# Performance work log

Measured on AMD Instinct MI355X. Metric: run time of the kernel, lower is better.

## Reference

```python
import jax, jax.numpy as jnp
import numpy as np

N = 8192      # number of tokens (input_dim in the original code)
D = 512       # hidden/embedding dim
R = 20        # number of dependency labels (2R with reverses)
L = 2         # num_layers
OUT = 256     # output_dim


def setup_inputs() -> dict:
    key = jax.random.key(0)
    ks = jax.random.split(key, 10)
    s = 0.02
    return {
        "x": jax.random.normal(ks[0], (N, D), dtype=jnp.float32),
        "dep_idx": jax.random.randint(ks[1], (N,), 0, N, dtype=jnp.int32),
        "rel_idx": jax.random.randint(ks[2], (N,), 0, R, dtype=jnp.int32),
        "gov_idx": jax.random.randint(ks[3], (N,), 0, N, dtype=jnp.int32),
        "W_self": jax.random.normal(ks[4], (L, D, D), dtype=jnp.float32) * s,
        "b_self": jax.random.normal(ks[5], (L, D), dtype=jnp.float32) * s,
        "W_rel": jax.random.normal(ks[6], (L, 2 * R, D, D), dtype=jnp.float32) * s,
        "b_rel": jax.random.normal(ks[7], (L, 2 * R, D), dtype=jnp.float32) * s,
        "W_ff": jax.random.normal(ks[8], (OUT, D), dtype=jnp.float32) * s,
        "b_ff": jax.random.normal(ks[9], (OUT,), dtype=jnp.float32) * s,
    }


def _gcn_layer(x, dep_idx, rel_idx, gov_idx, Ws, bs, Wr, br):
    # self transform applied to every token: temp[idx] = W_self @ x[idx] + b
    out = x @ Ws.T + bs  # [N, D]
    # relation-specific message passing: loop over the small fixed label set.
    # For each relation r: transform ALL nodes once (dense GEMM), then
    # mask-gather-scatter only the edges carrying that relation.
    for r in range(R):
        m = (rel_idx == r)[:, None]                      # [E, 1]
        # forward direction: dependent += W_r @ x[governor] + b_r
        h_f = x @ Wr[r].T + br[r]                        # [N, D]
        out = out.at[dep_idx].add(jnp.where(m, h_f[gov_idx], 0.0))
        # reverse direction: governor += W_{r}_r @ x[dependent] + b
        h_b = x @ Wr[R + r].T + br[R + r]                # [N, D]
        out = out.at[gov_idx].add(jnp.where(m, h_b[dep_idx], 0.0))
    return jax.nn.relu(out)


def reference(x, dep_idx, rel_idx, gov_idx, W_self, b_self, W_rel, b_rel, W_ff, b_ff):
    h = x
    for l in range(L):  # dropout_rate=0.0 -> dropout is identity; last layer has no dropout anyway
        h = _gcn_layer(h, dep_idx, rel_idx, gov_idx, W_self[l], b_self[l], W_rel[l], b_rel[l])
    return h @ W_ff.T + b_ff  # [N, OUT]
```

## Files before the change

kernel.cpp:

```cpp
#include <hip/hip_runtime.h>

#define N_TOK 8192
#define DIM   512
#define NREL  20
#define NGRP  40
#define OUTD  256
#define STILE 64
#define MAXT  168
#define MAXP  (MAXT*128)

typedef unsigned short u16;
typedef u16    u16x8  __attribute__((ext_vector_type(8)));
typedef __bf16 bf16x8 __attribute__((ext_vector_type(8)));
typedef float  f32x4  __attribute__((ext_vector_type(4)));

__device__ __forceinline__ u16 f2bf(float f) {
  union { float f; unsigned u; } v; v.f = f;
  return (u16)((v.u + 0x7FFFu + ((v.u >> 16) & 1u)) >> 16);
}

__global__ void k_cvt4(const float* __restrict__ s0, u16* __restrict__ d0, int m0,
                       const float* __restrict__ s1, u16* __restrict__ d1, int m1,
                       const float* __restrict__ s2, u16* __restrict__ d2, int m2,
                       const float* __restrict__ s3, u16* __restrict__ d3, int m3) {
  const int stride = gridDim.x * blockDim.x;
  const int t0 = blockIdx.x * blockDim.x + threadIdx.x;
#define CVT_LOOP(S, D, N)                                                    \
  for (int i = t0; i < N; i += stride) {                                     \
    float4 v = reinterpret_cast<const float4*>(S)[i];                        \
    reinterpret_cast<ushort4*>(D)[i] =                                       \
        make_ushort4(f2bf(v.x), f2bf(v.y), f2bf(v.z), f2bf(v.w));            \
  }
  CVT_LOOP(s0, d0, m0) CVT_LOOP(s1, d1, m1) CVT_LOOP(s2, d2, m2) CVT_LOOP(s3, d3, m3)
#undef CVT_LOOP
}

__global__ void k_cvtr(const float* __restrict__ in, u16* __restrict__ out, int n4) {
  const int stride = gridDim.x * blockDim.x;
  for (int i = blockIdx.x * blockDim.x + threadIdx.x; i < n4; i += stride) {
    float4 v = reinterpret_cast<const float4*>(in)[i];
    reinterpret_cast<ushort4*>(out)[i] =
        make_ushort4(f2bf(fmaxf(v.x, 0.f)), f2bf(fmaxf(v.y, 0.f)),
                     f2bf(fmaxf(v.z, 0.f)), f2bf(fmaxf(v.w, 0.f)));
  }
}

__global__ void k_prep(const int* __restrict__ rel, int* __restrict__ po,
                       int* __restrict__ segtab, int* __restrict__ cur) {
  __shared__ int hist[NREL];
  __shared__ int tpo[NGRP + 1];
  const int t = threadIdx.x;
  if (t < NREL) { hist[t] = 0; cur[t] = 0; }
  __syncthreads();
  for (int e = t; e < N_TOK; e += 256) atomicAdd(&hist[rel[e]], 1);
  __syncthreads();
  if (t == 0) {
    int acc = 0;
    for (int s = 0; s < NGRP; ++s) {
      int r = (s < NREL) ? s : s - NREL;
      tpo[s] = acc;
      acc += (hist[r] + 127) >> 7;
    }
    tpo[NGRP] = acc;
  }
  __syncthreads();
  if (t <= NGRP) po[t] = tpo[t] << 7;
  if (t < MAXT) {
    int s = -1;
    if (t < tpo[NGRP]) {
      int lo = 0, hi = NGRP - 1;
      while (lo < hi) { int mid = (lo + hi + 1) >> 1; if (tpo[mid] <= t) lo = mid; else hi = mid - 1; }
      s = lo;
    }
    segtab[t] = s;
  }
}

__global__ void k_fill2(const int* __restrict__ rel, const int* __restrict__ dep,
                        const int* __restrict__ gov, const int* __restrict__ po,
                        int* __restrict__ cur, int* __restrict__ msrc,
                        int* __restrict__ mdst) {
  int e = blockIdx.x * blockDim.x + threadIdx.x;
  if (e < N_TOK) {
    int r = rel[e];
    int p = atomicAdd(&cur[r], 1);
    int pf = po[r] + p, pb = po[NREL + r] + p;
    msrc[pf] = gov[e]; mdst[pf] = dep[e];
    msrc[pb] = dep[e]; mdst[pb] = gov[e];
  }
}

template <int KIND>
__global__ __launch_bounds__(256) void k_mm(
    const u16* __restrict__ A,
    const u16* __restrict__ Wself, const u16* __restrict__ Wrel,
    const float* __restrict__ bself, const float* __restrict__ brel,
    const int* __restrict__ msrc, const int* __restrict__ mdst,
    const int* __restrict__ segtab,
    float* __restrict__ Cf, int Nn)
{
  bool isSelf = true;
  int me0 = 0;
  const u16* Bsrc = Wself;
  const float* bb = bself;
  if (KIND == 2 && blockIdx.x >= STILE) {
    isSelf = false;
    const int et = blockIdx.x - STILE;
    const int seg = segtab[et];
    if (seg < 0) return;
    me0 = et * 128;
    Bsrc = Wrel + (size_t)seg * DIM * DIM;
    bb = brel + (size_t)seg * DIM;
  }
  const int m0 = blockIdx.x * 128;
  const int n0 = blockIdx.y * 128;

  __shared__ u16 As[128 * 64];
  __shared__ u16 Bs[128 * 64];

  const int t = threadIdx.x, w = t >> 6, l = t & 63;
  const int wm = (w >> 1) * 64, wn = (w & 1) * 64;
  const int lc = l & 15, h8 = l >> 4;
  const int wch = (t & 7) ^ ((t >> 3) & 7);

  const u16* gApt[4]; const u16* gBpt[4]; bool azero[4];
#pragma unroll
  for (int p = 0; p < 4; ++p) {
    const int row = p * 32 + (t >> 3);
    int arow;
    if (KIND == 2 && !isSelf) { arow = msrc[me0 + row]; azero[p] = (arow < 0); if (arow < 0) arow = 0; }
    else { arow = m0 + row; azero[p] = false; }
    gApt[p] = A + (size_t)arow * DIM + (t & 7) * 8;
    gBpt[p] = Bsrc + (size_t)(n0 + row) * DIM + (t & 7) * 8;
  }

  f32x4 acc[4][4] = {};

  for (int k0 = 0; k0 < DIM; k0 += 64) {
#pragma unroll
    for (int p = 0; p < 4; ++p) {
      const int row = p * 32 + (t >> 3);
      u16x8 av = {0, 0, 0, 0, 0, 0, 0, 0};
      if (!azero[p]) av = *reinterpret_cast<const u16x8*>(gApt[p] + k0);
      *reinterpret_cast<u16x8*>(&As[row * 64 + wch * 8]) = av;
      u16x8 bw = *reinterpret_cast<const u16x8*>(gBpt[p] + k0);
      *reinterpret_cast<u16x8*>(&Bs[row * 64 + wch * 8]) = bw;
    }
    __syncthreads();
#pragma unroll
    for (int ks = 0; ks < 2; ++ks) {
      const int rc = ks * 4 + h8;
      bf16x8 af[4], bfr[4];
#pragma unroll
      for (int mi = 0; mi < 4; ++mi)
        af[mi] = *reinterpret_cast<const bf16x8*>(&As[(wm + mi * 16 + lc) * 64 + (rc ^ (lc & 7)) * 8]);
#pragma unroll
      for (int ni = 0; ni < 4; ++ni)
        bfr[ni] = *reinterpret_cast<const bf16x8*>(&Bs[(wn + ni * 16 + lc) * 64 + (rc ^ (lc & 7)) * 8]);
#pragma unroll
      for (int mi = 0; mi < 4; ++mi)
#pragma unroll
        for (int ni = 0; ni < 4; ++ni)
          acc[mi][ni] = __builtin_amdgcn_mfma_f32_16x16x32_bf16(af[mi], bfr[ni], acc[mi][ni], 0, 0, 0);
    }
    __syncthreads();
  }

  float bv[4];
#pragma unroll
  for (int ni = 0; ni < 4; ++ni) bv[ni] = bb[n0 + wn + ni * 16 + lc];

#pragma unroll
  for (int mi = 0; mi < 4; ++mi)
#pragma unroll
    for (int j = 0; j < 4; ++j) {
      const int rloc = wm + mi * 16 + h8 * 4 + j;
      if (KIND == 2) {
        int dst;
        if (isSelf) dst = m0 + rloc;
        else { dst = mdst[me0 + rloc]; if (dst < 0) continue; }
        float* pout = Cf + (size_t)dst * DIM + n0 + wn + lc;
#pragma unroll
        for (int ni = 0; ni < 4; ++ni)
          unsafeAtomicAdd(pout + ni * 16, acc[mi][ni][j] + bv[ni]);
      } else {
        float* pout = Cf + (size_t)(m0 + rloc) * Nn + n0 + wn + lc;
#pragma unroll
        for (int ni = 0; ni < 4; ++ni)
          pout[ni * 16] = acc[mi][ni][j] + bv[ni];
      }
    }
}

extern "C" void kernel_launch(void* const* d_in, const int* in_sizes, int n_in,
                              void* d_out, int out_size, void* d_ws, size_t ws_size,
                              hipStream_t stream) {
  const float* x      = (const float*)d_in[0];
  const int*   dep    = (const int*)d_in[1];
  const int*   rel    = (const int*)d_in[2];
  const int*   gov    = (const int*)d_in[3];
  const float* W_self = (const float*)d_in[4];
  const float* b_self = (const float*)d_in[5];
  const float* W_rel  = (const float*)d_in[6];
  const float* b_rel  = (const float*)d_in[7];
  const float* W_ff   = (const float*)d_in[8];
  const float* b_ff   = (const float*)d_in[9];
  float* out = (float*)d_out;

  char* ws = (char*)d_ws;
  size_t o = 0;
  auto alloc = [&](size_t bytes) -> void* {
    void* p = ws + o;
    o = (o + bytes + 255) & ~(size_t)255;
    return p;
  };
  u16*   Wrel_bf  = (u16*)alloc((size_t)2 * NGRP * DIM * DIM * 2);
  u16*   Wself_bf = (u16*)alloc((size_t)2 * DIM * DIM * 2);
  u16*   Wff_bf   = (u16*)alloc((size_t)OUTD * DIM * 2);
  u16*   hb0      = (u16*)alloc((size_t)N_TOK * DIM * 2);
  u16*   hb1      = (u16*)alloc((size_t)N_TOK * DIM * 2);
  float* outf     = (float*)alloc((size_t)N_TOK * DIM * 4);
  int*   po       = (int*)alloc((NGRP + 1) * 4);
  int*   cur      = (int*)alloc(NREL * 4);
  int*   msrc     = (int*)alloc(MAXP * 4);
  int*   mdst     = (int*)alloc(MAXP * 4);
  int*   segtab   = (int*)alloc(MAXT * 4);
  (void)ws_size; (void)in_sizes; (void)n_in; (void)out_size;

  k_cvt4<<<2048, 256, 0, stream>>>(
      W_rel, Wrel_bf, 2 * NGRP * DIM * DIM / 4,
      W_self, Wself_bf, 2 * DIM * DIM / 4,
      W_ff, Wff_bf, OUTD * DIM / 4,
      x, hb0, N_TOK * DIM / 4);

  hipMemsetAsync(msrc, 0xFF, (size_t)2 * MAXP * 4, stream);
  k_prep<<<1, 256, 0, stream>>>(rel, po, segtab, cur);
  k_fill2<<<N_TOK / 256, 256, 0, stream>>>(rel, dep, gov, po, cur, msrc, mdst);

  u16* hin = hb0;
  u16* hout = hb1;
  for (int l = 0; l < 2; ++l) {
    hipMemsetAsync(outf, 0, (size_t)N_TOK * DIM * 4, stream);
    k_mm<2><<<dim3(STILE + MAXT, DIM / 128), 256, 0, stream>>>(
        hin,
        Wself_bf + (size_t)l * DIM * DIM,
        Wrel_bf + (size_t)l * NGRP * DIM * DIM,
        b_self + (size_t)l * DIM,
        b_rel + (size_t)l * NGRP * DIM,
        msrc, mdst, segtab, outf, DIM);
    k_cvtr<<<2048, 256, 0, stream>>>(outf, hout, N_TOK * DIM / 4);
    u16* tmp = hin; hin = hout; hout = tmp;
  }

  k_mm<0><<<dim3(STILE, OUTD / 128), 256, 0, stream>>>(
      hin, Wff_bf, nullptr, b_ff, nullptr, nullptr, nullptr, nullptr, out, OUTD);
}
```

Baseline: 371.4 us.

## Use direct global-to-LDS loads in GEMM and fold memsets into existing kernels

The GEMM tile loads now use global_load_lds to write 16-byte chunks straight into LDS, bypassing registers. The XOR swizzle moves to the global address side, and padded edge rows now point at row 0 with mdst=-1 instead of being zero-filled. The separate hipMemsetAsync calls are removed: the fp32 accumulator zeroing is folded into the conversion kernels using two ping-pong buffers, and padding initialisation moves into k_prep. This cuts launch count and register staging, but padded rows now do real loads, and correctness depends on the epilogue skipping mdst<0.

```diff
diff --git a/kernel.cpp b/kernel.cpp
--- a/kernel.cpp
+++ b/kernel.cpp
@@ -19,10 +19,17 @@
   return (u16)((v.u + 0x7FFFu + ((v.u >> 16) & 1u)) >> 16);
 }
 
+__device__ __forceinline__ void gl16(const void* g, void* l) {
+  __builtin_amdgcn_global_load_lds(
+      (const __attribute__((address_space(1))) void*)g,
+      (__attribute__((address_space(3))) void*)l, 16, 0, 0);
+}
+
 __global__ void k_cvt4(const float* __restrict__ s0, u16* __restrict__ d0, int m0,
                        const float* __restrict__ s1, u16* __restrict__ d1, int m1,
                        const float* __restrict__ s2, u16* __restrict__ d2, int m2,
-                       const float* __restrict__ s3, u16* __restrict__ d3, int m3) {
+                       const float* __restrict__ s3, u16* __restrict__ d3, int m3,
+                       float4* __restrict__ z, int nz) {
   const int stride = gridDim.x * blockDim.x;
   const int t0 = blockIdx.x * blockDim.x + threadIdx.x;
 #define CVT_LOOP(S, D, N)                                                    \
@@ -33,20 +40,29 @@
   }
   CVT_LOOP(s0, d0, m0) CVT_LOOP(s1, d1, m1) CVT_LOOP(s2, d2, m2) CVT_LOOP(s3, d3, m3)
 #undef CVT_LOOP
-}
-
-__global__ void k_cvtr(const float* __restrict__ in, u16* __restrict__ out, int n4) {
+  const float4 zero = make_float4(0.f, 0.f, 0.f, 0.f);
+  for (int i = t0; i < nz; i += stride) z[i] = zero;
+}
+
+__global__ void k_cvtr(const float* __restrict__ in, u16* __restrict__ out,
+                       float4* __restrict__ z, int n4) {
   const int stride = gridDim.x * blockDim.x;
-  for (int i = blockIdx.x * blockDim.x + threadIdx.x; i < n4; i += stride) {
+  const int t0 = blockIdx.x * blockDim.x + threadIdx.x;
+  for (int i = t0; i < n4; i += stride) {
     float4 v = reinterpret_cast<const float4*>(in)[i];
     reinterpret_cast<ushort4*>(out)[i] =
         make_ushort4(f2bf(fmaxf(v.x, 0.f)), f2bf(fmaxf(v.y, 0.f)),
                      f2bf(fmaxf(v.z, 0.f)), f2bf(fmaxf(v.w, 0.f)));
   }
+  if (z != nullptr) {
+    const float4 zero = make_float4(0.f, 0.f, 0.f, 0.f);
+    for (int i = t0; i < n4; i += stride) z[i] = zero;
+  }
 }
 
 __global__ void k_prep(const int* __restrict__ rel, int* __restrict__ po,
-                       int* __restrict__ segtab, int* __restrict__ cur) {
+                       int* __restrict__ segtab, int* __restrict__ cur,
+                       int* __restrict__ msrc, int* __restrict__ mdst) {
   __shared__ int hist[NREL];
   __shared__ int tpo[NGRP + 1];
   const int t = threadIdx.x;
@@ -68,11 +84,17 @@
   if (t < MAXT) {
     int s = -1;
     if (t < tpo[NGRP]) {
-      int lo = 0, hi = NGRP - 1;
-      while (lo < hi) { int mid = (lo + hi + 1) >> 1; if (tpo[mid] <= t) lo = mid; else hi = mid - 1; }
-      s = lo;
+      s = 0;
+      for (int q = 1; q < NGRP; ++q) if (tpo[q] <= t) s = q;
     }
     segtab[t] = s;
+  }
+  __syncthreads();
+  for (int s = 0; s < NGRP; ++s) {
+    const int r = (s < NREL) ? s : s - NREL;
+    const int start = (tpo[s] << 7) + hist[r];
+    const int end   = tpo[s + 1] << 7;
+    for (int i = start + t; i < end; i += 256) { msrc[i] = 0; mdst[i] = -1; }
   }
 }
 
@@ -121,17 +143,17 @@
   const int t = threadIdx.x, w = t >> 6, l = t & 63;
   const int wm = (w >> 1) * 64, wn = (w & 1) * 64;
   const int lc = l & 15, h8 = l >> 4;
-  const int wch = (t & 7) ^ ((t >> 3) & 7);
-
-  const u16* gApt[4]; const u16* gBpt[4]; bool azero[4];
+  const int chunk = (t & 7) ^ ((t >> 3) & 7);
+
+  const u16* gApt[4]; const u16* gBpt[4];
 #pragma unroll
   for (int p = 0; p < 4; ++p) {
     const int row = p * 32 + (t >> 3);
     int arow;
-    if (KIND == 2 && !isSelf) { arow = msrc[me0 + row]; azero[p] = (arow < 0); if (arow < 0) arow = 0; }
-    else { arow = m0 + row; azero[p] = false; }
-    gApt[p] = A + (size_t)arow * DIM + (t & 7) * 8;
-    gBpt[p] = Bsrc + (size_t)(n0 + row) * DIM + (t & 7) * 8;
+    if (KIND == 2 && !isSelf) arow = msrc[me0 + row];
+    else arow = m0 + row;
+    gApt[p] = A + (size_t)arow * DIM + chunk * 8;
+    gBpt[p] = Bsrc + (size_t)(n0 + row) * DIM + chunk * 8;
   }
 
   f32x4 acc[4][4] = {};
@@ -139,12 +161,10 @@
   for (int k0 = 0; k0 < DIM; k0 += 64) {
 #pragma unroll
     for (int p = 0; p < 4; ++p) {
-      const int row = p * 32 + (t >> 3);
-      u16x8 av = {0, 0, 0, 0, 0, 0, 0, 0};
-      if (!azero[p]) av = *reinterpret_cast<const u16x8*>(gApt[p] + k0);
-      *reinterpret_cast<u16x8*>(&As[row * 64 + wch * 8]) = av;
-      u16x8 bw = *reinterpret_cast<const u16x8*>(gBpt[p] + k0);
-      *reinterpret_cast<u16x8*>(&Bs[row * 64 + wch * 8]) = bw;
+      const unsigned lofs =
+          (unsigned)__builtin_amdgcn_readfirstlane((p * 32 + w * 8) * 128);
+      gl16(gApt[p] + k0, (char*)As + lofs);
+      gl16(gBpt[p] + k0, (char*)Bs + lofs);
     }
     __syncthreads();
 #pragma unroll
@@ -219,7 +239,8 @@
   u16*   Wff_bf   = (u16*)alloc((size_t)OUTD * DIM * 2);
   u16*   hb0      = (u16*)alloc((size_t)N_TOK * DIM * 2);
   u16*   hb1      = (u16*)alloc((size_t)N_TOK * DIM * 2);
-  float* outf     = (float*)alloc((size_t)N_TOK * DIM * 4);
+  float* outf0    = (float*)alloc((size_t)N_TOK * DIM * 4);
+  float* outf1    = (float*)alloc((size_t)N_TOK * DIM * 4);
   int*   po       = (int*)alloc((NGRP + 1) * 4);
   int*   cur      = (int*)alloc(NREL * 4);
   int*   msrc     = (int*)alloc(MAXP * 4);
@@ -231,27 +252,18 @@
       W_rel, Wrel_bf, 2 * NGRP * DIM * DIM / 4,
       W_self, Wself_bf, 2 * DIM * DIM / 4,
       W_ff, Wff_bf, OUTD * DIM / 4,
-      x, hb0, N_TOK * DIM / 4);
-
-  hipMemsetAsync(msrc, 0xFF, (size_t)2 * MAXP * 4, stream);
-  k_prep<<<1, 256, 0, stream>>>(rel, po, segtab, cur);
+      x, hb0, N_TOK * DIM / 4,
+      (float4*)outf0, N_TOK * DIM / 4);
+  k_prep<<<1, 256, 0, stream>>>(rel, po, segtab, cur, msrc, mdst);
   k_fill2<<<N_TOK / 256, 256, 0, stream>>>(rel, dep, gov, po, cur, msrc, mdst);
 
-  u16* hin = hb0;
-  u16* hout = hb1;
-  for (int l = 0; l < 2; ++l) {
-    hipMemsetAsync(outf, 0, (size_t)N_TOK * DIM * 4, stream);
-    k_mm<2><<<dim3(STILE + MAXT, DIM / 128), 256, 0, stream>>>(
-        hin,
-        Wself_bf + (size_t)l * DIM * DIM,
-        Wrel_bf + (size_t)l * NGRP * DIM * DIM,
-        b_self + (size_t)l * DIM,
-        b_rel + (size_t)l * NGRP * DIM,
-        msrc, mdst, segtab, outf, DIM);
-    k_cvtr<<<2048, 256, 0, stream>>>(outf, hout, N_TOK * DIM / 4);
-    u16* tmp = hin; hin = hout; hout = tmp;
-  }
-
+  k_mm<2><<<dim3(STILE + MAXT, DIM / 128), 256, 0, stream>>>(
+      hb0, Wself_bf, Wrel_bf, b_self, b_rel, msrc, mdst, segtab, outf0, DIM);
+  k_cvtr<<<2048, 256, 0, stream>>>(outf0, hb1, (float4*)outf1, N_TOK * DIM / 4);
+  k_mm<2><<<dim3(STILE + MAXT, DIM / 128), 256, 0, stream>>>(
+      hb1, Wself_bf + (size_t)DIM * DIM, Wrel_bf + (size_t)NGRP * DIM * DIM,
+      b_self + DIM, b_rel + (size_t)NGRP * DIM, msrc, mdst, segtab, outf1, DIM);
+  k_cvtr<<<2048, 256, 0, stream>>>(outf1, hb0, nullptr, N_TOK * DIM / 4);
   k_mm<0><<<dim3(STILE, OUTD / 128), 256, 0, stream>>>(
-      hin, Wff_bf, nullptr, b_ff, nullptr, nullptr, nullptr, nullptr, out, OUTD);
-}
+      hb0, Wff_bf, nullptr, b_ff, nullptr, nullptr, nullptr, nullptr, out, OUTD);
+}
```

Measured after the change: 350.4 us. 5.7% less time.
